# Performance work log

Hardware: AMD Instinct MI355X
Metric: run time of the kernel (lower is better)

Reference implementation:

```python
import jax, jax.numpy as jnp
import numpy as np

T = 2048        # flattened tokens (one prefill sequence)
HID = 2048      # hidden_size
NH = 32         # query heads
NKV = 4         # kv heads
HD = 128        # head_dim
THETA = 1000000.0
EPS = 1e-6


def setup_inputs() -> dict:
    key = jax.random.key(0)
    k0, k1, k2 = jax.random.split(key, 3)
    return {
        "positions": jnp.arange(T, dtype=jnp.int32),
        "hidden_states": jax.random.normal(k0, (T, HID), dtype=jnp.float32),
        "w_qkv": jax.random.normal(k1, ((NH + 2 * NKV) * HD, HID), dtype=jnp.float32) * 0.02,
        "w_o": jax.random.normal(k2, (HID, NH * HD), dtype=jnp.float32) * 0.02,
        "q_norm_w": jnp.ones((HD,), dtype=jnp.float32),
        "k_norm_w": jnp.ones((HD,), dtype=jnp.float32),
    }


def _rmsnorm(x, w):
    # per-head RMSNorm over last dim (head_dim), fp32 math
    var = jnp.mean(x * x, axis=-1, keepdims=True)
    return x * jax.lax.rsqrt(var + EPS) * w


def _rope(x, positions):
    # NeoX-style rotary embedding over full head_dim
    d = x.shape[-1]
    inv_freq = 1.0 / (THETA ** (jnp.arange(0, d, 2, dtype=jnp.float32) / d))  # [d/2]
    ang = positions.astype(jnp.float32)[:, None] * inv_freq                   # [T, d/2]
    cos = jnp.cos(ang)[:, None, :]  # [T,1,d/2]
    sin = jnp.sin(ang)[:, None, :]
    x1, x2 = jnp.split(x, 2, axis=-1)
    return jnp.concatenate([x1 * cos - x2 * sin, x2 * cos + x1 * sin], axis=-1)


def reference(positions, hidden_states, w_qkv, w_o, q_norm_w, k_norm_w):
    # fused QKV projection (no bias)
    qkv = hidden_states @ w_qkv.T                       # [T, (NH+2*NKV)*HD]
    q, k, v = jnp.split(qkv, [NH * HD, (NH + NKV) * HD], axis=-1)
    q = _rmsnorm(q.reshape(T, NH, HD), q_norm_w)        # [T,NH,HD]
    k = _rmsnorm(k.reshape(T, NKV, HD), k_norm_w)       # [T,NKV,HD]
    v = v.reshape(T, NKV, HD)
    q = _rope(q, positions)
    k = _rope(k, positions)
    # GQA: expand kv heads to query heads
    g = NH // NKV
    k = jnp.repeat(k, g, axis=1)                        # [T,NH,HD]
    v = jnp.repeat(v, g, axis=1)
    scale = HD ** -0.5
    scores = jnp.einsum('qhd,khd->hqk', q, k) * scale   # [NH,T,T]
    causal = jnp.tril(jnp.ones((T, T), dtype=bool))
    scores = jnp.where(causal[None, :, :], scores, jnp.finfo(scores.dtype).min)
    attn = jax.nn.softmax(scores, axis=-1)
    o = jnp.einsum('hqk,khd->qhd', attn, v).reshape(T, NH * HD)
    return o @ w_o.T                                    # [T,HID]
```

## Files before the change

### kernel.cpp

```cpp
#include <hip/hip_runtime.h>
#include <math.h>

#define T 2048
#define HID 2048
#define NH 32
#define NKV 4
#define HD 128
#define QKV_DIM 5120
#define OD 4096
#define VOFF 4608
#define C2LOG 0.12751743f
#define MFIX 6.0f

typedef _Float16 half8 __attribute__((ext_vector_type(8)));
typedef _Float16 half4v __attribute__((ext_vector_type(4)));
typedef float floatx4 __attribute__((ext_vector_type(4)));
typedef float floatx16 __attribute__((ext_vector_type(16)));
typedef unsigned uint4v __attribute__((ext_vector_type(4)));

#define GLD16(gp, lp) __builtin_amdgcn_global_load_lds( \
    (const __attribute__((address_space(1))) void*)(gp), \
    (__attribute__((address_space(3))) void*)(lp), 16, 0, 0)

__device__ __forceinline__ unsigned pk_u32(float a, float b) {
    auto h = __builtin_amdgcn_cvt_pkrtz(a, b);
    return __builtin_bit_cast(unsigned, h);
}
__device__ __forceinline__ void plswap(unsigned &a, unsigned &b) {
    asm("v_permlane32_swap_b32 %0, %1" : "+v"(a), "+v"(b));
}

__global__ __launch_bounds__(256)
void cvt_all(const float* __restrict__ h, const float* __restrict__ wq,
             const float* __restrict__ wo, _Float16* __restrict__ out) {
    size_t i = ((size_t)blockIdx.x * 256 + threadIdx.x) * 4;
    const float* src;
    size_t off;
    if (i < (size_t)T * HID)                        { src = h;  off = i; }
    else if (i < (size_t)T * HID + (size_t)QKV_DIM * HID)
                                                    { src = wq; off = i - (size_t)T * HID; }
    else                                            { src = wo; off = i - (size_t)T * HID - (size_t)QKV_DIM * HID; }
    float4 v = *(const float4*)(src + off);
    half4v o = { (_Float16)v.x, (_Float16)v.y, (_Float16)v.z, (_Float16)v.w };
    *(half4v*)(out + i) = o;
}

__global__ __launch_bounds__(256)
void gemm_sk_h(const _Float16* __restrict__ A, const _Float16* __restrict__ B,
               _Float16* __restrict__ p0, _Float16* __restrict__ p1,
               int M, int N, int K, int KS) {
    __shared__ __align__(16) _Float16 Asm[8192];
    __shared__ __align__(16) _Float16 Bsm[8192];
    int tid = threadIdx.x;
    int wave = tid >> 6, lane = tid & 63;
    int quad = lane >> 4, l16 = lane & 15;
    int m0 = blockIdx.y * 128, n0 = blockIdx.x * 128;
    int koff = blockIdx.z * KS;
    _Float16* C = blockIdx.z ? p1 : p0;
    int wm = (wave >> 1) * 64, wn = (wave & 1) * 64;
    const _Float16* Ag = A + (size_t)(m0 + (tid >> 2)) * K + koff + (tid & 3) * 8;
    const _Float16* Bg = B + (size_t)(n0 + (tid >> 2)) * K + koff + (tid & 3) * 8;
    size_t row64 = (size_t)64 * K;
    int wofs = wave * 512;
    floatx4 acc[4][4] = {};
    int nt = KS >> 5;
    GLD16(Ag, Asm + wofs);
    GLD16(Ag + row64, Asm + 2048 + wofs);
    GLD16(Bg, Bsm + wofs);
    GLD16(Bg + row64, Bsm + 2048 + wofs);
    for (int t = 0; t < nt; t++) {
        int cur = t & 1;
        if (t + 1 < nt) {
            const _Float16* Agp = Ag + (size_t)(t + 1) * 32;
            const _Float16* Bgp = Bg + (size_t)(t + 1) * 32;
            int nb = (cur ^ 1) * 4096 + wofs;
            GLD16(Agp, Asm + nb);
            GLD16(Agp + row64, Asm + nb + 2048);
            GLD16(Bgp, Bsm + nb);
            GLD16(Bgp + row64, Bsm + nb + 2048);
            asm volatile("s_waitcnt vmcnt(4)" ::: "memory");
        } else {
            asm volatile("s_waitcnt vmcnt(0)" ::: "memory");
        }
        __builtin_amdgcn_s_barrier();
        __builtin_amdgcn_sched_barrier(0);
        int pb = cur * 4096;
        half8 af[4], bf[4];
        #pragma unroll
        for (int i = 0; i < 4; i++)
            af[i] = *(const half8*)&Asm[pb + (wm + i * 16 + l16) * 32 + quad * 8];
        #pragma unroll
        for (int j = 0; j < 4; j++)
            bf[j] = *(const half8*)&Bsm[pb + (wn + j * 16 + l16) * 32 + quad * 8];
        #pragma unroll
        for (int i = 0; i < 4; i++)
            #pragma unroll
            for (int j = 0; j < 4; j++)
                acc[i][j] = __builtin_amdgcn_mfma_f32_16x16x32_f16(af[i], bf[j], acc[i][j], 0, 0, 0);
        __builtin_amdgcn_s_barrier();
    }
    #pragma unroll
    for (int i = 0; i < 4; i++) {
        int row = m0 + wm + i * 16 + quad * 4;
        #pragma unroll
        for (int j = 0; j < 4; j++) {
            int col = n0 + wn + j * 16 + l16;
            #pragma unroll
            for (int r = 0; r < 4; r++)
                C[(size_t)(row + r) * N + col] = (_Float16)acc[i][j][r];
        }
    }
}

__global__ __launch_bounds__(256)
void reduce2(const _Float16* __restrict__ p0, const _Float16* __restrict__ p1,
             float* __restrict__ out) {
    size_t i = ((size_t)blockIdx.x * 256 + threadIdx.x) * 4;
    half4v a = *(const half4v*)(p0 + i);
    half4v b = *(const half4v*)(p1 + i);
    float4 o = { (float)a.x + (float)b.x, (float)a.y + (float)b.y,
                 (float)a.z + (float)b.z, (float)a.w + (float)b.w };
    *(float4*)(out + i) = o;
}

__global__ __launch_bounds__(256)
void qkv_post(const _Float16* __restrict__ qp0, const _Float16* __restrict__ qp1,
              const int* __restrict__ positions,
              const float* __restrict__ qw, const float* __restrict__ kw,
              _Float16* __restrict__ Qb, _Float16* __restrict__ Kb) {
    int t = blockIdx.x;
    int wave = threadIdx.x >> 6, lane = threadIdx.x & 63;
    float pos = (float)positions[t];
    float f = exp2f(-(float)lane * (19.9315685693241741f / 64.0f));
    float ang = pos * f;
    float s = sinf(ang), c = cosf(ang);
    const _Float16* r0 = qp0 + (size_t)t * QKV_DIM;
    const _Float16* r1 = qp1 + (size_t)t * QKV_DIM;
    for (int hh = wave; hh < NH + NKV; hh += 4) {
        float x1 = (float)r0[hh * HD + lane] + (float)r1[hh * HD + lane];
        float x2 = (float)r0[hh * HD + lane + 64] + (float)r1[hh * HD + lane + 64];
        float ss = x1 * x1 + x2 * x2;
        for (int o = 1; o < 64; o <<= 1) ss += __shfl_xor(ss, o);
        float inv = rsqrtf(ss * (1.0f / HD) + 1e-6f);
        const float* w = (hh < NH) ? qw : kw;
        x1 = x1 * inv * w[lane];
        x2 = x2 * inv * w[lane + 64];
        float y1 = x1 * c - x2 * s;
        float y2 = x2 * c + x1 * s;
        _Float16* dst;
        if (hh < NH) dst = Qb + ((size_t)hh * T + t) * HD;
        else         dst = Kb + ((size_t)(hh - NH) * T + t) * HD;
        dst[lane]      = (_Float16)y1;
        dst[lane + 64] = (_Float16)y2;
    }
}

__global__ __launch_bounds__(256)
void v_trans(const _Float16* __restrict__ qp0, const _Float16* __restrict__ qp1,
             _Float16* __restrict__ Vt) {
    __shared__ _Float16 Ls[64][72];
    int tz = blockIdx.x & 31, dz = blockIdx.x >> 5;
    int tid = threadIdx.x;
    int rr = tid >> 3, c8 = (tid & 7) * 8;
    #pragma unroll
    for (int it = 0; it < 2; it++) {
        int row = it * 32 + rr;
        size_t src = (size_t)(tz * 64 + row) * QKV_DIM + VOFF + dz * 64 + c8;
        half8 a = *(const half8*)(qp0 + src);
        half8 b = *(const half8*)(qp1 + src);
        half8 sv;
        #pragma unroll
        for (int e = 0; e < 8; e++) sv[e] = (_Float16)((float)a[e] + (float)b[e]);
        *(half8*)&Ls[row][c8] = sv;
    }
    __syncthreads();
    #pragma unroll
    for (int it = 0; it < 2; it++) {
        int d = it * 32 + rr;
        half8 o;
        #pragma unroll
        for (int e = 0; e < 8; e++) o[e] = Ls[c8 + e][d];
        *(half8*)(Vt + (size_t)(dz * 64 + d) * T + tz * 64 + c8) = o;
    }
}

__global__ __launch_bounds__(256, 2)
void attn(const _Float16* __restrict__ Qb, const _Float16* __restrict__ Kb,
          const _Float16* __restrict__ Vt, _Float16* __restrict__ Ob) {
    __shared__ __align__(16) _Float16 Ksm[8192];
    __shared__ __align__(16) _Float16 Vsm[8192];
    int b = blockIdx.x;
    int halfg = b >> 8;
    int idx = b & 255;
    int h = idx & 31;
    int qi = idx >> 5;
    int j = halfg ? qi : 15 - qi;
    int hk = h >> 3;
    int tid = threadIdx.x, wave = tid >> 6, lane = tid & 63;
    int l31 = lane & 31, hi = lane >> 5;
    int wq0 = j * 128 + wave * 32;
    int qa = wq0 + l31;

    half8 qf[8];
    {
        const _Float16* qp = Qb + ((size_t)h * T + qa) * HD + hi * 8;
        #pragma unroll
        for (int kb = 0; kb < 8; kb++)
            qf[kb] = *(const half8*)(qp + kb * 16);
    }
    floatx16 o_acc[4] = {};
    float lsum = 0.0f;

    int krow = tid >> 4;
    const _Float16* Kg = Kb + ((size_t)hk * T + krow) * HD + ((tid & 15) ^ (krow & 7)) * 8;
    int vrow = tid >> 3;
    const _Float16* Vg = Vt + ((size_t)hk * HD + vrow) * T + ((tid & 7) ^ (vrow & 7)) * 8;
    _Float16* KsmW = Ksm + wave * 512;
    _Float16* VsmW = Vsm + wave * 512;

    int ntiles = 2 * j + 2;
    for (int it = 0; it < ntiles; it++) {
        int kv0 = it * 64;
        __syncthreads();
        {
            const _Float16* kg = Kg + (size_t)kv0 * HD;
            const _Float16* vg = Vg + kv0;
            #pragma unroll
            for (int c = 0; c < 4; c++) {
                GLD16(kg + (size_t)c * (16 * HD), KsmW + c * 2048);
                GLD16(vg + (size_t)c * (32 * T), VsmW + c * 2048);
            }
        }
        __syncthreads();

        bool needmask = (it >= ntiles - 2);
        half8 af[4];
        #pragma unroll
        for (int s = 0; s < 2; s++) {
            int row = s * 32 + l31;
            int rs = row & 7;
            floatx16 sc = {};
            #pragma unroll
            for (int kb = 0; kb < 8; kb++) {
                half8 kf = *(const half8*)&Ksm[row * 128 + (((kb * 2 + hi) ^ rs)) * 8];
                sc = __builtin_amdgcn_mfma_f32_32x32x16_f16(kf, qf[kb], sc, 0, 0, 0);
            }
            float pe[16];
            #pragma unroll
            for (int r = 0; r < 16; r++) {
                float p = __builtin_amdgcn_exp2f(
                    __builtin_fmaf(sc[r], C2LOG, -MFIX));
                if (needmask) {
                    int kv = kv0 + s * 32 + (r & 3) + 8 * (r >> 2) + 4 * hi;
                    p = (kv <= qa) ? p : 0.0f;
                }
                lsum += p;
                pe[r] = p;
            }
            #pragma unroll
            for (int c = 0; c < 2; c++) {
                int rb = c * 8;
                unsigned x0 = pk_u32(pe[rb + 0], pe[rb + 1]);
                unsigned y0 = pk_u32(pe[rb + 4], pe[rb + 5]);
                plswap(x0, y0);
                unsigned x1 = pk_u32(pe[rb + 2], pe[rb + 3]);
                unsigned y1 = pk_u32(pe[rb + 6], pe[rb + 7]);
                plswap(x1, y1);
                uint4v w = { x0, x1, y0, y1 };
                af[s * 2 + c] = __builtin_bit_cast(half8, w);
            }
        }
        #pragma unroll
        for (int db = 0; db < 4; db++) {
            int row = db * 32 + l31;
            int rs = row & 7;
            #pragma unroll
            for (int c = 0; c < 4; c++) {
                half8 vf = *(const half8*)&Vsm[row * 64 + (((c * 2 + hi) ^ rs)) * 8];
                o_acc[db] = __builtin_amdgcn_mfma_f32_32x32x16_f16(af[c], vf, o_acc[db], 0, 0, 0);
            }
        }
    }

    lsum += __shfl_xor(lsum, 32);
    float linv = 1.0f / lsum;
    float li[16];
    #pragma unroll
    for (int r = 0; r < 16; r++) {
        int rq = (r & 3) + 8 * (r >> 2) + 4 * hi;
        li[r] = __shfl(linv, rq);
    }
    #pragma unroll
    for (int db = 0; db < 4; db++) {
        int col = h * HD + db * 32 + l31;
        #pragma unroll
        for (int r = 0; r < 16; r++) {
            int rq = (r & 3) + 8 * (r >> 2) + 4 * hi;
            Ob[(size_t)(wq0 + rq) * OD + col] = (_Float16)(o_acc[db][r] * li[r]);
        }
    }
}

extern "C" void kernel_launch(void* const* d_in, const int* in_sizes, int n_in,
                              void* d_out, int out_size, void* d_ws, size_t ws_size,
                              hipStream_t stream) {
    const int*   positions = (const int*)d_in[0];
    const float* hidden    = (const float*)d_in[1];
    const float* w_qkv     = (const float*)d_in[2];
    const float* w_o       = (const float*)d_in[3];
    const float* q_norm_w  = (const float*)d_in[4];
    const float* k_norm_w  = (const float*)d_in[5];
    float* out = (float*)d_out;

    const size_t MiB = 1048576;
    char* ws = (char*)d_ws;
    _Float16* hb    = (_Float16*)(ws);
    _Float16* wqkvb = (_Float16*)(ws + 8 * MiB);
    _Float16* wob   = (_Float16*)(ws + 28 * MiB);
    _Float16* qkvp0 = (_Float16*)(ws + 44 * MiB);
    _Float16* qkvp1 = (_Float16*)(ws + 64 * MiB);
    _Float16* Qb    = (_Float16*)(ws + 84 * MiB);
    _Float16* Kb    = (_Float16*)(ws + 100 * MiB);
    _Float16* Vt    = (_Float16*)(ws + 102 * MiB);
    _Float16* Ob    = (_Float16*)(ws + 104 * MiB);
    _Float16* op0   = (_Float16*)(ws);
    _Float16* op1   = (_Float16*)(ws + 9 * MiB);

    cvt_all<<<22528, 256, 0, stream>>>(hidden, w_qkv, w_o, hb);

    gemm_sk_h<<<dim3(QKV_DIM / 128, T / 128, 2), 256, 0, stream>>>(
        hb, wqkvb, qkvp0, qkvp1, T, QKV_DIM, HID, HID / 2);

    qkv_post<<<T, 256, 0, stream>>>(qkvp0, qkvp1, positions, q_norm_w, k_norm_w, Qb, Kb);
    v_trans<<<256, 256, 0, stream>>>(qkvp0, qkvp1, Vt);

    attn<<<512, 256, 0, stream>>>(Qb, Kb, Vt, Ob);

    gemm_sk_h<<<dim3(HID / 128, T / 128, 2), 256, 0, stream>>>(
        Ob, wob, op0, op1, T, HID, OD, OD / 2);
    reduce2<<<T * HID / 1024, 256, 0, stream>>>(op0, op1, out);
}
```

Baseline: 330.5 us.

## Use 256x256 GEMM tiles with triple-buffered LDS, swizzle, and 4-way split-K

Replaces the 128x128 split-K GEMM with a 512-thread 256x256 tile kernel. It uses a three-stage LDS pipeline, an XOR swizzle against bank conflicts, interleaved prefetch between MFMA halves and s_setprio. The output projection now splits K four ways with a 4-input reduction, which adds partial-buffer traffic. Larger tiles raise reuse but leave fewer blocks (80 and 256) to fill the CUs, and 96KB LDS per block limits occupancy.

```diff
diff --git a/kernel.cpp b/kernel.cpp
--- a/kernel.cpp
+++ b/kernel.cpp
@@ -45,81 +45,119 @@
     *(half4v*)(out + i) = o;
 }
 
-__global__ __launch_bounds__(256)
-void gemm_sk_h(const _Float16* __restrict__ A, const _Float16* __restrict__ B,
-               _Float16* __restrict__ p0, _Float16* __restrict__ p1,
-               int M, int N, int K, int KS) {
-    __shared__ __align__(16) _Float16 Asm[8192];
-    __shared__ __align__(16) _Float16 Bsm[8192];
+__global__ __launch_bounds__(512, 2)
+void gemm8(const _Float16* __restrict__ A, const _Float16* __restrict__ B,
+           _Float16* __restrict__ p0, _Float16* __restrict__ p1,
+           _Float16* __restrict__ p2, _Float16* __restrict__ p3,
+           int M, int N, int K, int KS) {
+    __shared__ __align__(16) _Float16 sa[3][8192];
+    __shared__ __align__(16) _Float16 sb[3][8192];
     int tid = threadIdx.x;
     int wave = tid >> 6, lane = tid & 63;
     int quad = lane >> 4, l16 = lane & 15;
-    int m0 = blockIdx.y * 128, n0 = blockIdx.x * 128;
-    int koff = blockIdx.z * KS;
-    _Float16* C = blockIdx.z ? p1 : p0;
-    int wm = (wave >> 1) * 64, wn = (wave & 1) * 64;
-    const _Float16* Ag = A + (size_t)(m0 + (tid >> 2)) * K + koff + (tid & 3) * 8;
-    const _Float16* Bg = B + (size_t)(n0 + (tid >> 2)) * K + koff + (tid & 3) * 8;
-    size_t row64 = (size_t)64 * K;
+    int m0 = blockIdx.y * 256, n0 = blockIdx.x * 256;
+    int bz = blockIdx.z;
+    _Float16* C = (bz == 0) ? p0 : (bz == 1) ? p1 : (bz == 2) ? p2 : p3;
+    int koff = bz * KS;
+    int wm = (wave >> 2) * 128;
+    int wn = (wave & 3) * 64;
+    int srow = tid >> 2;
+    int scs = (tid & 3) ^ ((srow >> 1) & 3);
+    const _Float16* Ag = A + (size_t)(m0 + srow) * K + koff + scs * 8;
+    const _Float16* Bg = B + (size_t)(n0 + srow) * K + koff + scs * 8;
+    size_t row128 = (size_t)128 * K;
     int wofs = wave * 512;
-    floatx4 acc[4][4] = {};
-    int nt = KS >> 5;
-    GLD16(Ag, Asm + wofs);
-    GLD16(Ag + row64, Asm + 2048 + wofs);
-    GLD16(Bg, Bsm + wofs);
-    GLD16(Bg + row64, Bsm + 2048 + wofs);
-    for (int t = 0; t < nt; t++) {
-        int cur = t & 1;
-        if (t + 1 < nt) {
-            const _Float16* Agp = Ag + (size_t)(t + 1) * 32;
-            const _Float16* Bgp = Bg + (size_t)(t + 1) * 32;
-            int nb = (cur ^ 1) * 4096 + wofs;
-            GLD16(Agp, Asm + nb);
-            GLD16(Agp + row64, Asm + nb + 2048);
-            GLD16(Bgp, Bsm + nb);
-            GLD16(Bgp + row64, Bsm + nb + 2048);
-            asm volatile("s_waitcnt vmcnt(4)" ::: "memory");
-        } else {
-            asm volatile("s_waitcnt vmcnt(0)" ::: "memory");
-        }
+    int rc = (quad ^ ((l16 >> 1) & 3)) * 8;
+    int NT = KS >> 5;
+
+    floatx4 acc[8][4] = {};
+
+    #pragma unroll
+    for (int g0 = 0; g0 < 2; g0++) {
+        const _Float16* ag = Ag + (size_t)g0 * 32;
+        const _Float16* bg = Bg + (size_t)g0 * 32;
+        GLD16(ag,          sa[g0] + wofs);
+        GLD16(ag + row128, sa[g0] + 4096 + wofs);
+        GLD16(bg,          sb[g0] + wofs);
+        GLD16(bg + row128, sb[g0] + 4096 + wofs);
+    }
+
+    for (int g = 0; g < NT; ++g) {
+        int s = g % 3;
+        bool pre = (g + 2 < NT);
+        int s2 = (g + 2) % 3;
+        const _Float16* sA = sa[s];
+        const _Float16* sB = sb[s];
+        if (g + 1 < NT) asm volatile("s_waitcnt vmcnt(4)" ::: "memory");
+        else            asm volatile("s_waitcnt vmcnt(0)" ::: "memory");
         __builtin_amdgcn_s_barrier();
+        half8 af[4], bf[4];
+        #pragma unroll
+        for (int j = 0; j < 4; j++)
+            bf[j] = *(const half8*)&sB[(wn + j * 16 + l16) * 32 + rc];
+        #pragma unroll
+        for (int ii = 0; ii < 4; ii++)
+            af[ii] = *(const half8*)&sA[(wm + ii * 16 + l16) * 32 + rc];
+        if (pre) {
+            const _Float16* ag = Ag + (size_t)(g + 2) * 32;
+            GLD16(ag,          sa[s2] + wofs);
+            GLD16(ag + row128, sa[s2] + 4096 + wofs);
+        }
+        asm volatile("s_waitcnt lgkmcnt(0)" ::: "memory");
         __builtin_amdgcn_sched_barrier(0);
-        int pb = cur * 4096;
-        half8 af[4], bf[4];
-        #pragma unroll
-        for (int i = 0; i < 4; i++)
-            af[i] = *(const half8*)&Asm[pb + (wm + i * 16 + l16) * 32 + quad * 8];
-        #pragma unroll
-        for (int j = 0; j < 4; j++)
-            bf[j] = *(const half8*)&Bsm[pb + (wn + j * 16 + l16) * 32 + quad * 8];
-        #pragma unroll
-        for (int i = 0; i < 4; i++)
+        __builtin_amdgcn_s_setprio(1);
+        #pragma unroll
+        for (int ii = 0; ii < 4; ii++)
             #pragma unroll
             for (int j = 0; j < 4; j++)
-                acc[i][j] = __builtin_amdgcn_mfma_f32_16x16x32_f16(af[i], bf[j], acc[i][j], 0, 0, 0);
+                acc[ii][j] = __builtin_amdgcn_mfma_f32_16x16x32_f16(af[ii], bf[j], acc[ii][j], 0, 0, 0);
+        __builtin_amdgcn_s_setprio(0);
         __builtin_amdgcn_s_barrier();
-    }
-    #pragma unroll
-    for (int i = 0; i < 4; i++) {
-        int row = m0 + wm + i * 16 + quad * 4;
+        #pragma unroll
+        for (int ii = 0; ii < 4; ii++)
+            af[ii] = *(const half8*)&sA[(wm + 64 + ii * 16 + l16) * 32 + rc];
+        if (pre) {
+            const _Float16* bg = Bg + (size_t)(g + 2) * 32;
+            GLD16(bg,          sb[s2] + wofs);
+            GLD16(bg + row128, sb[s2] + 4096 + wofs);
+        }
+        asm volatile("s_waitcnt lgkmcnt(0)" ::: "memory");
+        __builtin_amdgcn_sched_barrier(0);
+        __builtin_amdgcn_s_setprio(1);
+        #pragma unroll
+        for (int ii = 0; ii < 4; ii++)
+            #pragma unroll
+            for (int j = 0; j < 4; j++)
+                acc[4 + ii][j] = __builtin_amdgcn_mfma_f32_16x16x32_f16(af[ii], bf[j], acc[4 + ii][j], 0, 0, 0);
+        __builtin_amdgcn_s_setprio(0);
+    }
+
+    #pragma unroll
+    for (int ii = 0; ii < 8; ii++) {
+        int row = m0 + wm + (ii >> 2) * 64 + (ii & 3) * 16 + quad * 4;
         #pragma unroll
         for (int j = 0; j < 4; j++) {
             int col = n0 + wn + j * 16 + l16;
             #pragma unroll
             for (int r = 0; r < 4; r++)
-                C[(size_t)(row + r) * N + col] = (_Float16)acc[i][j][r];
+                C[(size_t)(row + r) * N + col] = (_Float16)acc[ii][j][r];
         }
     }
 }
 
 __global__ __launch_bounds__(256)
-void reduce2(const _Float16* __restrict__ p0, const _Float16* __restrict__ p1,
+void reduce4(const _Float16* __restrict__ p0, const _Float16* __restrict__ p1,
+             const _Float16* __restrict__ p2, const _Float16* __restrict__ p3,
              float* __restrict__ out) {
     size_t i = ((size_t)blockIdx.x * 256 + threadIdx.x) * 4;
     half4v a = *(const half4v*)(p0 + i);
     half4v b = *(const half4v*)(p1 + i);
-    float4 o = { (float)a.x + (float)b.x, (float)a.y + (float)b.y,
-                 (float)a.z + (float)b.z, (float)a.w + (float)b.w };
+    half4v c = *(const half4v*)(p2 + i);
+    half4v d = *(const half4v*)(p3 + i);
+    float4 o = { (float)a.x + (float)b.x + (float)c.x + (float)d.x,
+                 (float)a.y + (float)b.y + (float)c.y + (float)d.y,
+                 (float)a.z + (float)b.z + (float)c.z + (float)d.z,
+                 (float)a.w + (float)b.w + (float)c.w + (float)d.w };
     *(float4*)(out + i) = o;
 }
 
@@ -325,18 +363,20 @@
     _Float16* Ob    = (_Float16*)(ws + 104 * MiB);
     _Float16* op0   = (_Float16*)(ws);
     _Float16* op1   = (_Float16*)(ws + 9 * MiB);
+    _Float16* op2   = (_Float16*)(ws + 44 * MiB);
+    _Float16* op3   = (_Float16*)(ws + 53 * MiB);
 
     cvt_all<<<22528, 256, 0, stream>>>(hidden, w_qkv, w_o, hb);
 
-    gemm_sk_h<<<dim3(QKV_DIM / 128, T / 128, 2), 256, 0, stream>>>(
-        hb, wqkvb, qkvp0, qkvp1, T, QKV_DIM, HID, HID / 2);
+    gemm8<<<dim3(QKV_DIM / 256, T / 256, 2), 512, 0, stream>>>(
+        hb, wqkvb, qkvp0, qkvp1, qkvp0, qkvp1, T, QKV_DIM, HID, 1024);
 
     qkv_post<<<T, 256, 0, stream>>>(qkvp0, qkvp1, positions, q_norm_w, k_norm_w, Qb, Kb);
     v_trans<<<256, 256, 0, stream>>>(qkvp0, qkvp1, Vt);
 
     attn<<<512, 256, 0, stream>>>(Qb, Kb, Vt, Ob);
 
-    gemm_sk_h<<<dim3(HID / 128, T / 128, 2), 256, 0, stream>>>(
-        Ob, wob, op0, op1, T, HID, OD, OD / 2);
-    reduce2<<<T * HID / 1024, 256, 0, stream>>>(op0, op1, out);
-}
+    gemm8<<<dim3(HID / 256, T / 256, 4), 512, 0, stream>>>(
+        Ob, wob, op0, op1, op2, op3, T, HID, OD, 1024);
+    reduce4<<<T * HID / 1024, 256, 0, stream>>>(op0, op1, op2, op3, out);
+}
```

After: 333.3 us. No clear change (+0.9%).
